# Kernel optimization log

Measured on AMD Instinct MI355X. Metric: run time of the kernel, lower is better.

The kernel has to match this reference:

```python
import math
import jax, jax.numpy as jnp
import numpy as np

B, N, D_IN, D_MODEL, H, TOPK = 4, 2048, 256, 512, 8, 32
D_HEAD = D_MODEL // H
EPS = 1e-8


def _linear_params(key, fan_in, fan_out):
    lim = 1.0 / math.sqrt(fan_in)
    kw, kb = jax.random.split(key)
    W = jax.random.uniform(kw, (fan_in, fan_out), minval=-lim, maxval=lim, dtype=jnp.float32)
    b = jax.random.uniform(kb, (fan_out,), minval=-lim, maxval=lim, dtype=jnp.float32)
    return W, b


def setup_inputs() -> dict:
    key = jax.random.key(0)
    kx, ks, kq, kk, kv, ko = jax.random.split(key, 6)
    x = jax.random.normal(kx, (B, N, D_IN), dtype=jnp.float32)
    sim = jax.random.uniform(ks, (B, N, N), dtype=jnp.float32)  # non-negative similarity
    Wq, bq = _linear_params(kq, D_IN, D_MODEL)
    Wk, bk = _linear_params(kk, D_IN, D_MODEL)
    Wv, bv = _linear_params(kv, D_IN, D_MODEL)
    Wo, bo = _linear_params(ko, D_MODEL, D_MODEL)
    tau_raw = jnp.asarray(0.0, dtype=jnp.float32)
    return {"x": x, "sim": sim, "Wq": Wq, "bq": bq, "Wk": Wk, "bk": bk,
            "Wv": Wv, "bv": bv, "Wo": Wo, "bo": bo, "tau_raw": tau_raw}


def reference(x, sim, Wq, bq, Wk, bk, Wv, bv, Wo, bo, tau_raw):
    b, n, _ = x.shape
    # projections -> (B, H, N, d_head)
    def split_heads(t):
        return t.reshape(b, n, H, D_HEAD).transpose(0, 2, 1, 3)
    Qh = split_heads(x @ Wq + bq)
    Kh = split_heads(x @ Wk + bk)
    Vh = split_heads(x @ Wv + bv)

    # top-k masked, row-normalized similarity bias
    simc = jnp.maximum(sim, 0.0)
    diag = jnp.eye(n, dtype=bool)
    sim_for_topk = jnp.where(diag, -jnp.inf, simc)  # exclude self from top-k
    k = min(TOPK, n - 1)
    _, topk_idx = jax.lax.top_k(sim_for_topk, k)  # (B, N, k)
    bidx = jnp.arange(b)[:, None, None]
    ridx = jnp.arange(n)[None, :, None]
    keep = jnp.zeros((b, n, n), dtype=bool).at[bidx, ridx, topk_idx].set(True)
    keep = keep & ~diag
    sim_masked = jnp.where(keep, simc, 0.0)
    rowsum = jnp.maximum(sim_masked.sum(axis=-1, keepdims=True), EPS)
    sim_bias = sim_masked / rowsum  # (B, N, N), rows sum to 1 over kept entries

    tau = jax.nn.softplus(tau_raw)
    scale = 1.0 / math.sqrt(D_HEAD)
    logits = jnp.einsum('bhnd,bhmd->bhnm', Qh, Kh) * scale + tau * sim_bias[:, None, :, :]
    attn = jax.nn.softmax(logits, axis=-1)
    out = jnp.einsum('bhnm,bhmd->bhnd', attn, Vh)
    out = out.transpose(0, 2, 1, 3).reshape(b, n, D_MODEL)
    return out @ Wo + bo
```

## Files before the change

kernel.cpp:

```cpp
#include <hip/hip_runtime.h>

typedef unsigned int u32;
typedef unsigned short u16;
typedef unsigned long long u64;
typedef float f32x4 __attribute__((ext_vector_type(4)));
typedef u32 u32x4 __attribute__((ext_vector_type(4)));
typedef u32 u32x2 __attribute__((ext_vector_type(2)));

#define DEVINL static __device__ __forceinline__
#define LOG2E 1.44269504088896340736f
#define QSCALE 0.18033688011112042f

DEVINL u16 f2bf(float f) {
  u32 u = __builtin_bit_cast(u32, f);
  u32 r = u + 0x7FFFu + ((u >> 16) & 1u);
  return (u16)(r >> 16);
}

DEVINL u32 cvtpk(float lo, float hi) {
  u32 r;
  asm("v_cvt_pk_bf16_f32 %0, %1, %2" : "=v"(r) : "v"(lo), "v"(hi));
  return r;
}
DEVINL float exp2v(float x) {
  float r;
  asm("v_exp_f32 %0, %1" : "=v"(r) : "v"(x));
  return r;
}
DEVINL void mfma_b16(f32x4& c, u32x4 a, u32x4 b) {
  asm volatile("v_mfma_f32_16x16x32_bf16 %0, %1, %2, %0" : "+v"(c) : "v"(a), "v"(b));
}
DEVINL void mfma_fence() { asm volatile("s_nop 7\n\ts_nop 7"); }

DEVINL int mbcnt64(u64 m) {
  return __builtin_amdgcn_mbcnt_hi((u32)(m >> 32), __builtin_amdgcn_mbcnt_lo((u32)m, 0));
}
DEVINL u64 shfl_xor64(u64 v, int m) {
  u32 lo = (u32)v, hi = (u32)(v >> 32);
  lo = __shfl_xor(lo, m, 64);
  hi = __shfl_xor(hi, m, 64);
  return ((u64)hi << 32) | lo;
}

__global__ __launch_bounds__(256) void prep_kernel(
    const float* __restrict__ x, const float* __restrict__ Wq, const float* __restrict__ Wk,
    const float* __restrict__ Wv, const float* __restrict__ Wo, const float* __restrict__ bq,
    const float* __restrict__ bk, const float* __restrict__ bv, u16* __restrict__ xb,
    u16* __restrict__ WqkvT, u16* __restrict__ WoT, float* __restrict__ biasQKV) {
  __shared__ float T[64][65];
  const int blk = blockIdx.x, tid = threadIdx.x;
  if (blk < 1024) {
    int i0 = (blk * 256 + tid) * 8;
    f32x4 v0 = *(const f32x4*)(x + i0);
    f32x4 v1 = *(const f32x4*)(x + i0 + 4);
    u32x4 pk;
    pk[0] = (u32)f2bf(v0[0]) | ((u32)f2bf(v0[1]) << 16);
    pk[1] = (u32)f2bf(v0[2]) | ((u32)f2bf(v0[3]) << 16);
    pk[2] = (u32)f2bf(v1[0]) | ((u32)f2bf(v1[1]) << 16);
    pk[3] = (u32)f2bf(v1[2]) | ((u32)f2bf(v1[3]) << 16);
    *(u32x4*)(xb + i0) = pk;
    return;
  }
  if (blk < 1024 + 96 + 64) {
    int t = blk - 1024;
    const float* W;
    u16* dst;
    int k0, n0, outld, outrow0;
    if (t < 96) {
      int sel = t >> 5, tt = t & 31;
      W = sel == 0 ? Wq : (sel == 1 ? Wk : Wv);
      k0 = (tt >> 3) * 64;
      n0 = (tt & 7) * 64;
      dst = WqkvT;
      outld = 256;
      outrow0 = sel * 512 + n0;
    } else {
      int tt = t - 96;
      W = Wo;
      k0 = (tt >> 3) * 64;
      n0 = (tt & 7) * 64;
      dst = WoT;
      outld = 512;
      outrow0 = n0;
    }
    const int r = tid >> 2, q = tid & 3;
#pragma unroll
    for (int i = 0; i < 4; i++) {
      f32x4 vv = *(const f32x4*)(W + (size_t)(k0 + r) * 512 + n0 + q * 16 + i * 4);
      T[r][q * 16 + i * 4 + 0] = vv[0];
      T[r][q * 16 + i * 4 + 1] = vv[1];
      T[r][q * 16 + i * 4 + 2] = vv[2];
      T[r][q * 16 + i * 4 + 3] = vv[3];
    }
    __syncthreads();
    u16 tmpv[16];
#pragma unroll
    for (int e = 0; e < 16; e++) tmpv[e] = f2bf(T[q * 16 + e][r]);
    u32x4 w0, w1;
#pragma unroll
    for (int j = 0; j < 4; j++) {
      w0[j] = (u32)tmpv[2 * j] | ((u32)tmpv[2 * j + 1] << 16);
      w1[j] = (u32)tmpv[8 + 2 * j] | ((u32)tmpv[9 + 2 * j] << 16);
    }
    u16* dp = dst + (size_t)(outrow0 + r) * outld + k0 + q * 16;
    *(u32x4*)dp = w0;
    *(u32x4*)(dp + 8) = w1;
    return;
  }
  for (int i = tid; i < 1536; i += 256)
    biasQKV[i] = i < 512 ? bq[i] : (i < 1024 ? bk[i - 512] : bv[i - 1024]);
}

__global__ __launch_bounds__(256) void topk_kernel(const float* __restrict__ sim,
                                                   const float* __restrict__ tau_raw,
                                                   u32* __restrict__ tpw,
                                                   u32* __restrict__ tstarts) {
  __shared__ u32 keyA[4][64];
  __shared__ u32 idxA[4][64];
  const int tid = threadIdx.x, lane = tid & 63, w = tid >> 6;
  const int row = blockIdx.x * 4 + w;
  const int b = row >> 11, n = row & 2047;
  const float* src = sim + ((size_t)b * 2048 + n) * 2048;

  u32 keys[32];
#pragma unroll
  for (int q = 0; q < 8; q++) {
    f32x4 v = *(const f32x4*)(src + q * 256 + lane * 4);
#pragma unroll
    for (int j = 0; j < 4; j++) {
      int m = (q << 8) + lane * 4 + j;
      float xv = fmaxf(v[j], 0.f);
      keys[q * 4 + j] = (m == n) ? 0u : (__builtin_bit_cast(u32, xv) + 1u);
    }
  }

  u32 Plo = 1u;
  u32 Phi = 0x7F000000u;
  u32 P = 0x3F7C0001u;
  int c = 0;
  for (int it = 0; it < 40; ++it) {
    int lc = 0;
#pragma unroll
    for (int e = 0; e < 32; e++) lc += (keys[e] >= P) ? 1 : 0;
#pragma unroll
    for (int off = 1; off < 64; off <<= 1) lc += __shfl_xor(lc, off, 64);
    c = lc;
    if (c >= 32 && c <= 64) break;
    if (c < 32) Phi = P; else Plo = P;
    if (Phi - Plo <= 1) break;
    long long Pn;
    if (P >= 0x3F000000u && P <= 0x3F800000u) {
      Pn = (long long)P + (long long)(c - 48) * 4098;
    } else {
      Pn = (long long)Plo + (long long)((Phi - Plo) >> 1);
    }
    if (Pn <= (long long)Plo || Pn >= (long long)Phi)
      Pn = (long long)Plo + (long long)((Phi - Plo) >> 1);
    P = (u32)Pn;
  }

  u32* kws = keyA[w];
  u32* iws = idxA[w];
  int base = 0;
#pragma unroll
  for (int e = 0; e < 32; e++) {
    bool pred = keys[e] >= P;
    u64 mk = __ballot(pred);
    if (pred) {
      int slot = base + mbcnt64(mk);
      if (slot < 64) {
        kws[slot] = keys[e];
        iws[slot] = (u32)((e >> 2) * 256 + lane * 4 + (e & 3));
      }
    }
    base += __popcll(mk);
  }
  for (int s = base + lane; s < 64; s += 64) {
    kws[s] = 0u;
    iws[s] = 2047u;
  }

  u64 K = ((u64)kws[lane] << 11) | (u64)(2047u - iws[lane]);
#pragma unroll
  for (int k = 2; k <= 64; k <<= 1) {
#pragma unroll
    for (int j = k >> 1; j >= 1; j >>= 1) {
      u64 o = shfl_xor64(K, j);
      bool keepmax = (((lane & k) == 0) == ((lane & j) == 0));
      u64 mx = K > o ? K : o;
      u64 mn = K > o ? o : K;
      K = keepmax ? mx : mn;
    }
  }

  u32 key = (u32)(K >> 11);
  int myidx = 2047 - (int)(K & 0x7FFu);
  float myval = __builtin_bit_cast(float, key - 1u);
  float sv = (lane < 32) ? myval : 0.f;
#pragma unroll
  for (int off = 1; off < 64; off <<= 1) sv += __shfl_xor(sv, off, 64);
  float tau = log1pf(__expf(tau_raw[0]));
  float wvv = tau * myval / fmaxf(sv, 1e-8f) * LOG2E;

  int bucket = (myidx >> 2) & 3;
  u64 bm0 = __ballot(lane < 32 && bucket == 0);
  u64 bm1 = __ballot(lane < 32 && bucket == 1);
  u64 bm2 = __ballot(lane < 32 && bucket == 2);
  int c0 = __popcll(bm0), c1 = __popcll(bm1), c2 = __popcll(bm2);
  int key2 = (bucket << 11) | myidx;
  int rank = 0;
  for (int j2 = 0; j2 < 32; j2++) {
    int ok = __shfl(key2, j2, 64);
    rank += (ok < key2) ? 1 : 0;
  }
  if (lane < 32) tpw[(size_t)row * 32 + rank] = ((u32)myidx << 16) | (u32)f2bf(wvv);
  if (lane == 0)
    tstarts[row] = ((u32)c0 << 8) | ((u32)(c0 + c1) << 16) | ((u32)(c0 + c1 + c2) << 24);
}

template <int MODE>
__global__ __launch_bounds__(256) void gemm_nt(const u16* __restrict__ A,
                                               const u16* __restrict__ Bt,
                                               const float* __restrict__ bias,
                                               u16* __restrict__ outQ, u16* __restrict__ outK,
                                               u16* __restrict__ outV, float* __restrict__ outF,
                                               int M, int N, int K) {
  __shared__ __align__(16) u16 As[128 * 32];
  __shared__ __align__(16) u16 Bs[128 * 32];

  const int tid = threadIdx.x;
  const int lane = tid & 63;
  const int w = tid >> 6;
  const int g = lane >> 4, c = lane & 15;
  const int wr = (w >> 1) * 64, wc = (w & 1) * 64;
  const int m0 = blockIdx.y * 128, n0 = blockIdx.x * 128;

  f32x4 acc[4][4];
#pragma unroll
  for (int i = 0; i < 4; i++)
#pragma unroll
    for (int j = 0; j < 4; j++) acc[i][j] = f32x4{0.f, 0.f, 0.f, 0.f};

  const int srow = tid >> 1;
  const int shalf = tid & 1;
  const u16* Arow = A + (size_t)(m0 + srow) * K + shalf * 16;
  const u16* Brow = Bt + (size_t)(n0 + srow) * K + shalf * 16;
  char* asbase = (char*)As;
  char* bsbase = (char*)Bs;
  const u32 swz = (u32)((srow & 7) << 4);
  const u32 wb0 = (u32)(srow * 64 + shalf * 32);

  for (int kt = 0; kt < K; kt += 32) {
    __syncthreads();
    {
      u32x4 a0 = *(const u32x4*)(Arow + kt);
      u32x4 a1 = *(const u32x4*)(Arow + kt + 8);
      u32x4 b0 = *(const u32x4*)(Brow + kt);
      u32x4 b1 = *(const u32x4*)(Brow + kt + 8);
      *(u32x4*)(asbase + ((wb0 + 0) ^ swz)) = a0;
      *(u32x4*)(asbase + ((wb0 + 16) ^ swz)) = a1;
      *(u32x4*)(bsbase + ((wb0 + 0) ^ swz)) = b0;
      *(u32x4*)(bsbase + ((wb0 + 16) ^ swz)) = b1;
    }
    __syncthreads();
    u32x4 af[4], bfr[4];
#pragma unroll
    for (int fr = 0; fr < 4; fr++) {
      int row = wr + fr * 16 + c;
      af[fr] = *(const u32x4*)(asbase + ((u32)(row * 64 + g * 16) ^ ((u32)((row & 7) << 4))));
    }
#pragma unroll
    for (int fc = 0; fc < 4; fc++) {
      int row = wc + fc * 16 + c;
      bfr[fc] = *(const u32x4*)(bsbase + ((u32)(row * 64 + g * 16) ^ ((u32)((row & 7) << 4))));
    }
#pragma unroll
    for (int fr = 0; fr < 4; fr++)
#pragma unroll
      for (int fc = 0; fc < 4; fc++) mfma_b16(acc[fr][fc], af[fr], bfr[fc]);
  }
  mfma_fence();
#pragma unroll
  for (int fc = 0; fc < 4; fc++) {
    int gcol = n0 + wc + fc * 16 + c;
    float bvv = bias[gcol];
#pragma unroll
    for (int fr = 0; fr < 4; fr++) {
#pragma unroll
      for (int r = 0; r < 4; r++) {
        int grow = m0 + wr + fr * 16 + 4 * g + r;
        float v = acc[fr][fc][r] + bvv;
        if (MODE == 0) {
          int sel = gcol >> 9, c9 = gcol & 511;
          if (sel == 0) v *= QSCALE;
          int hh = c9 >> 6, dd = c9 & 63;
          int bb = grow >> 11, nn = grow & 2047;
          size_t off2 = ((size_t)(bb * 8 + hh) * 2048 + nn) * 64 + dd;
          u16* dst = sel == 0 ? outQ : (sel == 1 ? outK : outV);
          dst[off2] = f2bf(v);
        } else {
          outF[(size_t)grow * N + gcol] = v;
        }
      }
    }
  }
}

__global__ __launch_bounds__(256) void transpose_v(const u16* __restrict__ Vb,
                                                   u16* __restrict__ Vt) {
  __shared__ __align__(16) u16 T[64 * 72];
  const int nt = blockIdx.x, bh = blockIdx.y;
  const int tid = threadIdx.x;
  const int rr = tid >> 2, q = tid & 3;
  {
    const u16* src = Vb + ((size_t)bh * 2048 + nt * 64 + rr) * 64 + q * 16;
    u32x4 a = *(const u32x4*)src;
    u32x4 b = *(const u32x4*)(src + 8);
    *(u32x4*)(&T[rr * 72 + q * 16]) = a;
    *(u32x4*)(&T[rr * 72 + q * 16 + 8]) = b;
  }
  __syncthreads();
  {
    union { u16 s[16]; u32x4 v[2]; } ou;
#pragma unroll
    for (int e = 0; e < 16; e++) ou.s[e] = T[(q * 16 + e) * 72 + rr];
    u16* dst = Vt + ((size_t)bh * 64 + rr) * 2048 + nt * 64 + q * 16;
    *(u32x4*)dst = ou.v[0];
    *(u32x4*)(dst + 8) = ou.v[1];
  }
}

__global__ __launch_bounds__(256) void attn_kernel(const u16* __restrict__ Qb,
                                                   const u16* __restrict__ Kb,
                                                   const u16* __restrict__ Vt,
                                                   const u32* __restrict__ tpw,
                                                   const u32* __restrict__ tstarts,
                                                   u16* __restrict__ attnout) {
  __shared__ __align__(16) u16 Ks[64 * 64];
  __shared__ __align__(16) u16 Vs[64 * 64];
  __shared__ __align__(16) u16 Ps[4][16 * 64];
  __shared__ u32 pws[64 * 32];
  __shared__ u32 tst[64];

  const int bid = blockIdx.x;
  const int bh = (bid & 7) * 4 + ((bid >> 3) & 3);
  const int qt = bid >> 5;
  const int b = bh >> 3, h = bh & 7;
  const int tid = threadIdx.x, lane = tid & 63, w = tid >> 6;
  const int g = lane >> 4, c = lane & 15;
  const int qbase = qt * 64;

  for (int i = tid; i < 2048; i += 256)
    pws[i] = tpw[((size_t)b * 2048 + qbase) * 32 + i];
  if (tid < 64) tst[tid] = tstarts[b * 2048 + qbase + tid];

  const u16* qptr = Qb + ((size_t)bh * 2048 + qbase + w * 16 + c) * 64 + g * 8;
  u32x4 aq0 = *(const u32x4*)qptr;
  u32x4 aq1 = *(const u32x4*)(qptr + 32);

  float m = -1e30f, ssum = 0.f;
  f32x4 o[4];
#pragma unroll
  for (int db = 0; db < 4; db++) o[db] = f32x4{0.f, 0.f, 0.f, 0.f};

  const int rowl = w * 16 + c;

  const int sr = tid >> 2, sq = tid & 3;
  const u16* ksrc = Kb + ((size_t)bh * 2048 + sr) * 64 + sq * 16;
  const u16* vsrc = Vt + ((size_t)bh * 64 + sr) * 2048 + sq * 16;
  char* ksb = (char*)Ks;
  char* vsb = (char*)Vs;
  char* pwb = (char*)&Ps[w][0];
  const u32 sswz = (u32)((sr & 7) << 4);
  const u32 sb0 = (u32)(sr * 128 + sq * 32);

  u32 koff[4][2], poff2[2], pwoff[4][2];
#pragma unroll
  for (int cb = 0; cb < 4; cb++) {
    int row = cb * 16 + c;
    u32 sz = (u32)((row & 7) << 4);
    koff[cb][0] = ((u32)(row * 128 + g * 16)) ^ sz;
    koff[cb][1] = ((u32)(row * 128 + g * 16 + 64)) ^ sz;
  }
  {
    u32 sz = (u32)((c & 7) << 4);
#pragma unroll
    for (int mm = 0; mm < 2; mm++) poff2[mm] = ((u32)(c * 128 + mm * 64 + g * 16)) ^ sz;
#pragma unroll
    for (int cb = 0; cb < 4; cb++)
#pragma unroll
      for (int hh = 0; hh < 2; hh++)
        pwoff[cb][hh] = ((u32)(c * 128 + cb * 32 + g * 8 + hh * 4)) ^ sz;
  }

  __syncthreads();
  u32 stw = tst[rowl];
  int p = (int)((stw >> (8 * g)) & 255u);
  const int pend = (g == 3) ? 32 : (int)((stw >> (8 * g + 8)) & 255u);

  for (int jt = 0; jt < 2048; jt += 64) {
    __syncthreads();
    {
      u32x4 k0 = *(const u32x4*)(ksrc + (size_t)jt * 64);
      u32x4 k1 = *(const u32x4*)(ksrc + (size_t)jt * 64 + 8);
      u32x4 v0 = *(const u32x4*)(vsrc + jt);
      u32x4 v1 = *(const u32x4*)(vsrc + jt + 8);
      *(u32x4*)(ksb + ((sb0 + 0) ^ sswz)) = k0;
      *(u32x4*)(ksb + ((sb0 + 16) ^ sswz)) = k1;
      *(u32x4*)(vsb + ((sb0 + 0) ^ sswz)) = v0;
      *(u32x4*)(vsb + ((sb0 + 16) ^ sswz)) = v1;
    }
    __syncthreads();

    f32x4 s[4];
#pragma unroll
    for (int cb = 0; cb < 4; cb++) {
      u32x4 bk0 = *(const u32x4*)(ksb + koff[cb][0]);
      u32x4 bk1 = *(const u32x4*)(ksb + koff[cb][1]);
      f32x4 t = f32x4{0.f, 0.f, 0.f, 0.f};
      mfma_b16(t, bk0, aq0);
      mfma_b16(t, bk1, aq1);
      s[cb] = t;
    }
    mfma_fence();

    const int jtend = jt + 64;
    while (p < pend) {
      u32 e = pws[rowl * 32 + p];
      int j = (int)(e >> 16);
      if (j >= jtend) break;
      float wv = __builtin_bit_cast(float, e << 16);
      int rel = j - jt - 4 * g;
#pragma unroll
      for (int cb = 0; cb < 4; cb++)
#pragma unroll
        for (int r = 0; r < 4; r++) s[cb][r] += (rel == cb * 16 + r) ? wv : 0.f;
      p++;
    }

    float tm = fmaxf(fmaxf(fmaxf(s[0][0], s[0][1]), fmaxf(s[0][2], s[0][3])),
                     fmaxf(fmaxf(s[1][0], s[1][1]), fmaxf(s[1][2], s[1][3])));
    tm = fmaxf(tm, fmaxf(fmaxf(fmaxf(s[2][0], s[2][1]), fmaxf(s[2][2], s[2][3])),
                         fmaxf(fmaxf(s[3][0], s[3][1]), fmaxf(s[3][2], s[3][3]))));
    tm = fmaxf(tm, __shfl_xor(tm, 16, 64));
    tm = fmaxf(tm, __shfl_xor(tm, 32, 64));
    if (!__all(tm - m <= 8.f)) {
      float mn = fmaxf(m, tm);
      float f = exp2v(m - mn);
      m = mn;
      ssum *= f;
#pragma unroll
      for (int db = 0; db < 4; db++) o[db] *= f;
    }
    float lsum = 0.f;
#pragma unroll
    for (int cb = 0; cb < 4; cb++) {
      float e0 = exp2v(s[cb][0] - m);
      float e1 = exp2v(s[cb][1] - m);
      float e2 = exp2v(s[cb][2] - m);
      float e3 = exp2v(s[cb][3] - m);
      lsum += (e0 + e1) + (e2 + e3);
      *(u32*)(pwb + pwoff[cb][0]) = cvtpk(e0, e1);
      *(u32*)(pwb + pwoff[cb][1]) = cvtpk(e2, e3);
    }
    ssum += lsum;

    u32x4 pf0 = *(const u32x4*)(pwb + poff2[0]);
    u32x4 pf1 = *(const u32x4*)(pwb + poff2[1]);
#pragma unroll
    for (int db = 0; db < 4; db++) {
      u32x4 bv0 = *(const u32x4*)(vsb + koff[db][0]);
      u32x4 bv1 = *(const u32x4*)(vsb + koff[db][1]);
      mfma_b16(o[db], bv0, pf0);
      mfma_b16(o[db], bv1, pf1);
    }
    mfma_fence();
  }

  ssum += __shfl_xor(ssum, 16, 64);
  ssum += __shfl_xor(ssum, 32, 64);
  float inv = 1.f / ssum;
  const int n = qbase + w * 16 + c;
  u16* obase = attnout + ((size_t)b * 2048 + n) * 512 + h * 64 + 4 * g;
#pragma unroll
  for (int db = 0; db < 4; db++) {
    u32x2 st;
    st[0] = cvtpk(o[db][0] * inv, o[db][1] * inv);
    st[1] = cvtpk(o[db][2] * inv, o[db][3] * inv);
    *(u32x2*)(obase + db * 16) = st;
  }
}

extern "C" void kernel_launch(void* const* d_in, const int* in_sizes, int n_in,
                              void* d_out, int out_size, void* d_ws, size_t ws_size,
                              hipStream_t stream) {
  (void)in_sizes; (void)n_in; (void)out_size; (void)ws_size;
  const float* x = (const float*)d_in[0];
  const float* sim = (const float*)d_in[1];
  const float* Wq = (const float*)d_in[2];
  const float* bq = (const float*)d_in[3];
  const float* Wk = (const float*)d_in[4];
  const float* bk = (const float*)d_in[5];
  const float* Wv = (const float*)d_in[6];
  const float* bv = (const float*)d_in[7];
  const float* Wo = (const float*)d_in[8];
  const float* bo = (const float*)d_in[9];
  const float* tau = (const float*)d_in[10];
  float* out = (float*)d_out;

  char* ws = (char*)d_ws;
  size_t off = 0;
  auto alloc = [&](size_t bytes) {
    void* p = ws + off;
    off += (bytes + 255) & ~(size_t)255;
    return p;
  };
  u16* xb = (u16*)alloc((size_t)8192 * 256 * 2);
  u16* WqkvT = (u16*)alloc((size_t)1536 * 256 * 2);
  u16* WoT = (u16*)alloc((size_t)512 * 512 * 2);
  float* biasQKV = (float*)alloc((size_t)1536 * 4);
  u16* Qb = (u16*)alloc((size_t)32 * 2048 * 64 * 2);
  u16* Kb = (u16*)alloc((size_t)32 * 2048 * 64 * 2);
  u16* Vb = (u16*)alloc((size_t)32 * 2048 * 64 * 2);
  u16* Vt = (u16*)alloc((size_t)32 * 2048 * 64 * 2);
  u16* attnout = (u16*)alloc((size_t)8192 * 512 * 2);
  u32* tpw = (u32*)alloc((size_t)8192 * 32 * 4);
  u32* tstarts = (u32*)alloc((size_t)8192 * 4);

  prep_kernel<<<dim3(1185), dim3(256), 0, stream>>>(x, Wq, Wk, Wv, Wo, bq, bk, bv, xb, WqkvT,
                                                    WoT, biasQKV);
  topk_kernel<<<dim3(2048), dim3(256), 0, stream>>>(sim, tau, tpw, tstarts);
  gemm_nt<0><<<dim3(12, 64), dim3(256), 0, stream>>>(xb, WqkvT, biasQKV, Qb, Kb, Vb, nullptr,
                                                     8192, 1536, 256);
  transpose_v<<<dim3(32, 32), dim3(256), 0, stream>>>(Vb, Vt);
  attn_kernel<<<dim3(1024), dim3(256), 0, stream>>>(Qb, Kb, Vt, tpw, tstarts, attnout);
  gemm_nt<1><<<dim3(4, 64), dim3(256), 0, stream>>>(attnout, WoT, bo, nullptr, nullptr, nullptr,
                                                    out, 8192, 512, 512);
}
```

Measured before the change: 256.5 us.

## Double-buffer K/V tiles and process two query sub-tiles per attention block

The attention kernel now handles 128 query rows per block (two 64-row sub-tiles per wave), so each K/V tile loaded into shared memory is reused for twice as many queries. K/V staging becomes double-buffered with register prefetch two tiles ahead, which removes one barrier per iteration and overlaps global loads with MFMA work. The probability tile writes are also widened to 64-bit stores. The cost is more registers and shared memory per block and half as many blocks (512), which may lower occupancy and leave fewer blocks to spread across the GPU's CUs.

```diff
diff --git a/kernel.cpp b/kernel.cpp
--- a/kernel.cpp
+++ b/kernel.cpp
@@ -336,11 +336,11 @@
                                                    const u32* __restrict__ tpw,
                                                    const u32* __restrict__ tstarts,
                                                    u16* __restrict__ attnout) {
-  __shared__ __align__(16) u16 Ks[64 * 64];
-  __shared__ __align__(16) u16 Vs[64 * 64];
-  __shared__ __align__(16) u16 Ps[4][16 * 64];
-  __shared__ u32 pws[64 * 32];
-  __shared__ u32 tst[64];
+  __shared__ __align__(16) u16 Kd[2][64 * 64];
+  __shared__ __align__(16) u16 Vd[2][64 * 64];
+  __shared__ __align__(16) u16 Ps[4][2][16 * 64];
+  __shared__ u32 pws[128 * 32];
+  __shared__ u32 tst[128];
 
   const int bid = blockIdx.x;
   const int bh = (bid & 7) * 4 + ((bid >> 3) & 3);
@@ -348,33 +348,36 @@
   const int b = bh >> 3, h = bh & 7;
   const int tid = threadIdx.x, lane = tid & 63, w = tid >> 6;
   const int g = lane >> 4, c = lane & 15;
-  const int qbase = qt * 64;
-
-  for (int i = tid; i < 2048; i += 256)
+  const int qbase = qt * 128;
+
+  for (int i = tid; i < 4096; i += 256)
     pws[i] = tpw[((size_t)b * 2048 + qbase) * 32 + i];
-  if (tid < 64) tst[tid] = tstarts[b * 2048 + qbase + tid];
-
-  const u16* qptr = Qb + ((size_t)bh * 2048 + qbase + w * 16 + c) * 64 + g * 8;
-  u32x4 aq0 = *(const u32x4*)qptr;
-  u32x4 aq1 = *(const u32x4*)(qptr + 32);
-
-  float m = -1e30f, ssum = 0.f;
-  f32x4 o[4];
-#pragma unroll
-  for (int db = 0; db < 4; db++) o[db] = f32x4{0.f, 0.f, 0.f, 0.f};
-
-  const int rowl = w * 16 + c;
+  if (tid < 128) tst[tid] = tstarts[b * 2048 + qbase + tid];
+
+  u32x4 aq0[2], aq1[2];
+#pragma unroll
+  for (int s = 0; s < 2; s++) {
+    const u16* qptr = Qb + ((size_t)bh * 2048 + qbase + s * 64 + w * 16 + c) * 64 + g * 8;
+    aq0[s] = *(const u32x4*)qptr;
+    aq1[s] = *(const u32x4*)(qptr + 32);
+  }
+
+  float m[2] = {-1e30f, -1e30f}, ssum[2] = {0.f, 0.f};
+  f32x4 o[2][4];
+#pragma unroll
+  for (int s = 0; s < 2; s++)
+#pragma unroll
+    for (int db = 0; db < 4; db++) o[s][db] = f32x4{0.f, 0.f, 0.f, 0.f};
 
   const int sr = tid >> 2, sq = tid & 3;
   const u16* ksrc = Kb + ((size_t)bh * 2048 + sr) * 64 + sq * 16;
   const u16* vsrc = Vt + ((size_t)bh * 64 + sr) * 2048 + sq * 16;
-  char* ksb = (char*)Ks;
-  char* vsb = (char*)Vs;
-  char* pwb = (char*)&Ps[w][0];
+  char* ksbase = (char*)&Kd[0][0];
+  char* vsbase = (char*)&Vd[0][0];
   const u32 sswz = (u32)((sr & 7) << 4);
   const u32 sb0 = (u32)(sr * 128 + sq * 32);
 
-  u32 koff[4][2], poff2[2], pwoff[4][2];
+  u32 koff[4][2];
 #pragma unroll
   for (int cb = 0; cb < 4; cb++) {
     int row = cb * 16 + c;
@@ -382,112 +385,163 @@
     koff[cb][0] = ((u32)(row * 128 + g * 16)) ^ sz;
     koff[cb][1] = ((u32)(row * 128 + g * 16 + 64)) ^ sz;
   }
+  u32 poff2[2], pwoff[4];
   {
     u32 sz = (u32)((c & 7) << 4);
 #pragma unroll
     for (int mm = 0; mm < 2; mm++) poff2[mm] = ((u32)(c * 128 + mm * 64 + g * 16)) ^ sz;
 #pragma unroll
-    for (int cb = 0; cb < 4; cb++)
-#pragma unroll
-      for (int hh = 0; hh < 2; hh++)
-        pwoff[cb][hh] = ((u32)(c * 128 + cb * 32 + g * 8 + hh * 4)) ^ sz;
-  }
-
+    for (int cb = 0; cb < 4; cb++) pwoff[cb] = ((u32)(c * 128 + cb * 32 + g * 8)) ^ sz;
+  }
+
+  int p[2], pend[2];
+
+  u32x4 rk0 = *(const u32x4*)(ksrc);
+  u32x4 rk1 = *(const u32x4*)(ksrc + 8);
+  u32x4 rv0 = *(const u32x4*)(vsrc);
+  u32x4 rv1 = *(const u32x4*)(vsrc + 8);
+  *(u32x4*)(ksbase + ((sb0 + 0) ^ sswz)) = rk0;
+  *(u32x4*)(ksbase + ((sb0 + 16) ^ sswz)) = rk1;
+  *(u32x4*)(vsbase + ((sb0 + 0) ^ sswz)) = rv0;
+  *(u32x4*)(vsbase + ((sb0 + 16) ^ sswz)) = rv1;
+  rk0 = *(const u32x4*)(ksrc + 4096);
+  rk1 = *(const u32x4*)(ksrc + 4096 + 8);
+  rv0 = *(const u32x4*)(vsrc + 64);
+  rv1 = *(const u32x4*)(vsrc + 64 + 8);
   __syncthreads();
-  u32 stw = tst[rowl];
-  int p = (int)((stw >> (8 * g)) & 255u);
-  const int pend = (g == 3) ? 32 : (int)((stw >> (8 * g + 8)) & 255u);
-
-  for (int jt = 0; jt < 2048; jt += 64) {
+
+#pragma unroll
+  for (int s = 0; s < 2; s++) {
+    u32 stw = tst[s * 64 + w * 16 + c];
+    p[s] = (int)((stw >> (8 * g)) & 255u);
+    pend[s] = (g == 3) ? 32 : (int)((stw >> (8 * g + 8)) & 255u);
+  }
+
+  u32 curoff = 0;
+  for (int t = 0; t < 32; ++t) {
+    const int jt = t * 64;
+    {
+      u32 woff = curoff ^ 8192;
+      *(u32x4*)(ksbase + woff + ((sb0 + 0) ^ sswz)) = rk0;
+      *(u32x4*)(ksbase + woff + ((sb0 + 16) ^ sswz)) = rk1;
+      *(u32x4*)(vsbase + woff + ((sb0 + 0) ^ sswz)) = rv0;
+      *(u32x4*)(vsbase + woff + ((sb0 + 16) ^ sswz)) = rv1;
+    }
+    {
+      int jt2 = t < 30 ? (t + 2) * 64 : 1984;
+      const u16* kp = ksrc + (size_t)jt2 * 64;
+      const u16* vp = vsrc + jt2;
+      rk0 = *(const u32x4*)kp;
+      rk1 = *(const u32x4*)(kp + 8);
+      rv0 = *(const u32x4*)vp;
+      rv1 = *(const u32x4*)(vp + 8);
+    }
+
+    f32x4 sA[4], sB[4];
+#pragma unroll
+    for (int cb = 0; cb < 4; cb++) {
+      u32x4 bk0 = *(const u32x4*)(ksbase + curoff + koff[cb][0]);
+      u32x4 bk1 = *(const u32x4*)(ksbase + curoff + koff[cb][1]);
+      f32x4 tA = f32x4{0.f, 0.f, 0.f, 0.f};
+      f32x4 tB = f32x4{0.f, 0.f, 0.f, 0.f};
+      mfma_b16(tA, bk0, aq0[0]);
+      mfma_b16(tA, bk1, aq1[0]);
+      mfma_b16(tB, bk0, aq0[1]);
+      mfma_b16(tB, bk1, aq1[1]);
+      sA[cb] = tA;
+      sB[cb] = tB;
+    }
+    mfma_fence();
+
+    const int jtend = jt + 64;
+#pragma unroll
+    for (int s = 0; s < 2; s++) {
+      f32x4* sp = (s == 0) ? sA : sB;
+      const int rowl = s * 64 + w * 16 + c;
+      int pp = p[s];
+      const int pe = pend[s];
+      while (pp < pe) {
+        u32 e = pws[rowl * 32 + pp];
+        int j = (int)(e >> 16);
+        if (j >= jtend) break;
+        float wv = __builtin_bit_cast(float, e << 16);
+        int rel = j - jt - 4 * g;
+#pragma unroll
+        for (int cb = 0; cb < 4; cb++)
+#pragma unroll
+          for (int r = 0; r < 4; r++) sp[cb][r] += (rel == cb * 16 + r) ? wv : 0.f;
+        pp++;
+      }
+      p[s] = pp;
+
+      float tm = fmaxf(fmaxf(fmaxf(sp[0][0], sp[0][1]), fmaxf(sp[0][2], sp[0][3])),
+                       fmaxf(fmaxf(sp[1][0], sp[1][1]), fmaxf(sp[1][2], sp[1][3])));
+      tm = fmaxf(tm, fmaxf(fmaxf(fmaxf(sp[2][0], sp[2][1]), fmaxf(sp[2][2], sp[2][3])),
+                           fmaxf(fmaxf(sp[3][0], sp[3][1]), fmaxf(sp[3][2], sp[3][3]))));
+      tm = fmaxf(tm, __shfl_xor(tm, 16, 64));
+      tm = fmaxf(tm, __shfl_xor(tm, 32, 64));
+      if (!__all(tm - m[s] <= 8.f)) {
+        float mn = fmaxf(m[s], tm);
+        float f = exp2v(m[s] - mn);
+        m[s] = mn;
+        ssum[s] *= f;
+#pragma unroll
+        for (int db = 0; db < 4; db++) o[s][db] *= f;
+      }
+      char* pwb = (char*)&Ps[w][s][0];
+      float lsum = 0.f;
+#pragma unroll
+      for (int cb = 0; cb < 4; cb++) {
+        float e0 = exp2v(sp[cb][0] - m[s]);
+        float e1 = exp2v(sp[cb][1] - m[s]);
+        float e2 = exp2v(sp[cb][2] - m[s]);
+        float e3 = exp2v(sp[cb][3] - m[s]);
+        lsum += (e0 + e1) + (e2 + e3);
+        u32x2 pk;
+        pk[0] = cvtpk(e0, e1);
+        pk[1] = cvtpk(e2, e3);
+        *(u32x2*)(pwb + pwoff[cb]) = pk;
+      }
+      ssum[s] += lsum;
+    }
+
+    char* pwbA = (char*)&Ps[w][0][0];
+    char* pwbB = (char*)&Ps[w][1][0];
+    u32x4 pf0A = *(const u32x4*)(pwbA + poff2[0]);
+    u32x4 pf1A = *(const u32x4*)(pwbA + poff2[1]);
+    u32x4 pf0B = *(const u32x4*)(pwbB + poff2[0]);
+    u32x4 pf1B = *(const u32x4*)(pwbB + poff2[1]);
+
+#pragma unroll
+    for (int db = 0; db < 4; db++) {
+      u32x4 bv0 = *(const u32x4*)(vsbase + curoff + koff[db][0]);
+      u32x4 bv1 = *(const u32x4*)(vsbase + curoff + koff[db][1]);
+      mfma_b16(o[0][db], bv0, pf0A);
+      mfma_b16(o[0][db], bv1, pf1A);
+      mfma_b16(o[1][db], bv0, pf0B);
+      mfma_b16(o[1][db], bv1, pf1B);
+    }
+    mfma_fence();
+
     __syncthreads();
-    {
-      u32x4 k0 = *(const u32x4*)(ksrc + (size_t)jt * 64);
-      u32x4 k1 = *(const u32x4*)(ksrc + (size_t)jt * 64 + 8);
-      u32x4 v0 = *(const u32x4*)(vsrc + jt);
-      u32x4 v1 = *(const u32x4*)(vsrc + jt + 8);
-      *(u32x4*)(ksb + ((sb0 + 0) ^ sswz)) = k0;
-      *(u32x4*)(ksb + ((sb0 + 16) ^ sswz)) = k1;
-      *(u32x4*)(vsb + ((sb0 + 0) ^ sswz)) = v0;
-      *(u32x4*)(vsb + ((sb0 + 16) ^ sswz)) = v1;
-    }
-    __syncthreads();
-
-    f32x4 s[4];
-#pragma unroll
-    for (int cb = 0; cb < 4; cb++) {
-      u32x4 bk0 = *(const u32x4*)(ksb + koff[cb][0]);
-      u32x4 bk1 = *(const u32x4*)(ksb + koff[cb][1]);
-      f32x4 t = f32x4{0.f, 0.f, 0.f, 0.f};
-      mfma_b16(t, bk0, aq0);
-      mfma_b16(t, bk1, aq1);
-      s[cb] = t;
-    }
-    mfma_fence();
-
-    const int jtend = jt + 64;
-    while (p < pend) {
-      u32 e = pws[rowl * 32 + p];
-      int j = (int)(e >> 16);
-      if (j >= jtend) break;
-      float wv = __builtin_bit_cast(float, e << 16);
-      int rel = j - jt - 4 * g;
-#pragma unroll
-      for (int cb = 0; cb < 4; cb++)
-#pragma unroll
-        for (int r = 0; r < 4; r++) s[cb][r] += (rel == cb * 16 + r) ? wv : 0.f;
-      p++;
-    }
-
-    float tm = fmaxf(fmaxf(fmaxf(s[0][0], s[0][1]), fmaxf(s[0][2], s[0][3])),
-                     fmaxf(fmaxf(s[1][0], s[1][1]), fmaxf(s[1][2], s[1][3])));
-    tm = fmaxf(tm, fmaxf(fmaxf(fmaxf(s[2][0], s[2][1]), fmaxf(s[2][2], s[2][3])),
-                         fmaxf(fmaxf(s[3][0], s[3][1]), fmaxf(s[3][2], s[3][3]))));
-    tm = fmaxf(tm, __shfl_xor(tm, 16, 64));
-    tm = fmaxf(tm, __shfl_xor(tm, 32, 64));
-    if (!__all(tm - m <= 8.f)) {
-      float mn = fmaxf(m, tm);
-      float f = exp2v(m - mn);
-      m = mn;
-      ssum *= f;
-#pragma unroll
-      for (int db = 0; db < 4; db++) o[db] *= f;
-    }
-    float lsum = 0.f;
-#pragma unroll
-    for (int cb = 0; cb < 4; cb++) {
-      float e0 = exp2v(s[cb][0] - m);
-      float e1 = exp2v(s[cb][1] - m);
-      float e2 = exp2v(s[cb][2] - m);
-      float e3 = exp2v(s[cb][3] - m);
-      lsum += (e0 + e1) + (e2 + e3);
-      *(u32*)(pwb + pwoff[cb][0]) = cvtpk(e0, e1);
-      *(u32*)(pwb + pwoff[cb][1]) = cvtpk(e2, e3);
-    }
-    ssum += lsum;
-
-    u32x4 pf0 = *(const u32x4*)(pwb + poff2[0]);
-    u32x4 pf1 = *(const u32x4*)(pwb + poff2[1]);
+    curoff ^= 8192;
+  }
+
+#pragma unroll
+  for (int s = 0; s < 2; s++) {
+    float t = ssum[s];
+    t += __shfl_xor(t, 16, 64);
+    t += __shfl_xor(t, 32, 64);
+    float inv = 1.f / t;
+    const int n = qbase + s * 64 + w * 16 + c;
+    u16* obase = attnout + ((size_t)b * 2048 + n) * 512 + h * 64 + 4 * g;
 #pragma unroll
     for (int db = 0; db < 4; db++) {
-      u32x4 bv0 = *(const u32x4*)(vsb + koff[db][0]);
-      u32x4 bv1 = *(const u32x4*)(vsb + koff[db][1]);
-      mfma_b16(o[db], bv0, pf0);
-      mfma_b16(o[db], bv1, pf1);
-    }
-    mfma_fence();
-  }
-
-  ssum += __shfl_xor(ssum, 16, 64);
-  ssum += __shfl_xor(ssum, 32, 64);
-  float inv = 1.f / ssum;
-  const int n = qbase + w * 16 + c;
-  u16* obase = attnout + ((size_t)b * 2048 + n) * 512 + h * 64 + 4 * g;
-#pragma unroll
-  for (int db = 0; db < 4; db++) {
-    u32x2 st;
-    st[0] = cvtpk(o[db][0] * inv, o[db][1] * inv);
-    st[1] = cvtpk(o[db][2] * inv, o[db][3] * inv);
-    *(u32x2*)(obase + db * 16) = st;
+      u32x2 st;
+      st[0] = cvtpk(o[s][db][0] * inv, o[s][db][1] * inv);
+      st[1] = cvtpk(o[s][db][2] * inv, o[s][db][3] * inv);
+      *(u32x2*)(obase + db * 16) = st;
+    }
   }
 }
 
@@ -533,7 +587,7 @@
   gemm_nt<0><<<dim3(12, 64), dim3(256), 0, stream>>>(xb, WqkvT, biasQKV, Qb, Kb, Vb, nullptr,
                                                      8192, 1536, 256);
   transpose_v<<<dim3(32, 32), dim3(256), 0, stream>>>(Vb, Vt);
-  attn_kernel<<<dim3(1024), dim3(256), 0, stream>>>(Qb, Kb, Vt, tpw, tstarts, attnout);
+  attn_kernel<<<dim3(512), dim3(256), 0, stream>>>(Qb, Kb, Vt, tpw, tstarts, attnout);
   gemm_nt<1><<<dim3(4, 64), dim3(256), 0, stream>>>(attnout, WoT, bo, nullptr, nullptr, nullptr,
                                                     out, 8192, 512, 512);
 }
```

Measured after the change: 272.3 us. 1.06x slower.

## Prefetch next K/V tile into registers and stream top-k bias from global

Applied to the files above, without the earlier changes.

The attention loop now loads the next K/V tile into registers while the current tile is computed, so global latency overlaps with the MFMA and softmax work. The per-block shared-memory staging of top-k weights and start indices is removed; each lane instead reads its next sparse entry straight from global memory using a one-entry lookahead. It also merges two 32-bit P stores into one 64-bit store, adds s_setprio around the MFMA sections, and drops the fence after the PV MFMAs inside the loop. The trade-offs are higher register pressure from holding the prefetched tile and scattered global loads in the bias loop.

```diff
diff --git a/kernel.cpp b/kernel.cpp
--- a/kernel.cpp
+++ b/kernel.cpp
@@ -339,8 +339,6 @@
   __shared__ __align__(16) u16 Ks[64 * 64];
   __shared__ __align__(16) u16 Vs[64 * 64];
   __shared__ __align__(16) u16 Ps[4][16 * 64];
-  __shared__ u32 pws[64 * 32];
-  __shared__ u32 tst[64];
 
   const int bid = blockIdx.x;
   const int bh = (bid & 7) * 4 + ((bid >> 3) & 3);
@@ -349,21 +347,22 @@
   const int tid = threadIdx.x, lane = tid & 63, w = tid >> 6;
   const int g = lane >> 4, c = lane & 15;
   const int qbase = qt * 64;
-
-  for (int i = tid; i < 2048; i += 256)
-    pws[i] = tpw[((size_t)b * 2048 + qbase) * 32 + i];
-  if (tid < 64) tst[tid] = tstarts[b * 2048 + qbase + tid];
-
-  const u16* qptr = Qb + ((size_t)bh * 2048 + qbase + w * 16 + c) * 64 + g * 8;
+  const int rowl = w * 16 + c;
+
+  const u16* qptr = Qb + ((size_t)bh * 2048 + qbase + rowl) * 64 + g * 8;
   u32x4 aq0 = *(const u32x4*)qptr;
   u32x4 aq1 = *(const u32x4*)(qptr + 32);
 
+  const u32* tpwrow = tpw + ((size_t)b * 2048 + qbase + rowl) * 32;
+  u32 stw = tstarts[b * 2048 + qbase + rowl];
+  int p = (int)((stw >> (8 * g)) & 255u);
+  const int pend = (g == 3) ? 32 : (int)((stw >> (8 * g + 8)) & 255u);
+  u32 nextE = (p < pend) ? tpwrow[p] : 0xFFFF0000u;
+
   float m = -1e30f, ssum = 0.f;
   f32x4 o[4];
 #pragma unroll
   for (int db = 0; db < 4; db++) o[db] = f32x4{0.f, 0.f, 0.f, 0.f};
-
-  const int rowl = w * 16 + c;
 
   const int sr = tid >> 2, sq = tid & 3;
   const u16* ksrc = Kb + ((size_t)bh * 2048 + sr) * 64 + sq * 16;
@@ -374,7 +373,7 @@
   const u32 sswz = (u32)((sr & 7) << 4);
   const u32 sb0 = (u32)(sr * 128 + sq * 32);
 
-  u32 koff[4][2], poff2[2], pwoff[4][2];
+  u32 koff[4][2], poff2[2], pwoff[4];
 #pragma unroll
   for (int cb = 0; cb < 4; cb++) {
     int row = cb * 16 + c;
@@ -387,55 +386,57 @@
 #pragma unroll
     for (int mm = 0; mm < 2; mm++) poff2[mm] = ((u32)(c * 128 + mm * 64 + g * 16)) ^ sz;
 #pragma unroll
-    for (int cb = 0; cb < 4; cb++)
-#pragma unroll
-      for (int hh = 0; hh < 2; hh++)
-        pwoff[cb][hh] = ((u32)(c * 128 + cb * 32 + g * 8 + hh * 4)) ^ sz;
-  }
-
-  __syncthreads();
-  u32 stw = tst[rowl];
-  int p = (int)((stw >> (8 * g)) & 255u);
-  const int pend = (g == 3) ? 32 : (int)((stw >> (8 * g + 8)) & 255u);
-
-  for (int jt = 0; jt < 2048; jt += 64) {
+    for (int cb = 0; cb < 4; cb++) pwoff[cb] = ((u32)(c * 128 + cb * 32 + g * 8)) ^ sz;
+  }
+
+  u32x4 rk0 = *(const u32x4*)ksrc;
+  u32x4 rk1 = *(const u32x4*)(ksrc + 8);
+  u32x4 rv0 = *(const u32x4*)vsrc;
+  u32x4 rv1 = *(const u32x4*)(vsrc + 8);
+
+  for (int t = 0; t < 32; ++t) {
+    const int jt = t * 64;
     __syncthreads();
+    *(u32x4*)(ksb + ((sb0 + 0) ^ sswz)) = rk0;
+    *(u32x4*)(ksb + ((sb0 + 16) ^ sswz)) = rk1;
+    *(u32x4*)(vsb + ((sb0 + 0) ^ sswz)) = rv0;
+    *(u32x4*)(vsb + ((sb0 + 16) ^ sswz)) = rv1;
+    __syncthreads();
+
     {
-      u32x4 k0 = *(const u32x4*)(ksrc + (size_t)jt * 64);
-      u32x4 k1 = *(const u32x4*)(ksrc + (size_t)jt * 64 + 8);
-      u32x4 v0 = *(const u32x4*)(vsrc + jt);
-      u32x4 v1 = *(const u32x4*)(vsrc + jt + 8);
-      *(u32x4*)(ksb + ((sb0 + 0) ^ sswz)) = k0;
-      *(u32x4*)(ksb + ((sb0 + 16) ^ sswz)) = k1;
-      *(u32x4*)(vsb + ((sb0 + 0) ^ sswz)) = v0;
-      *(u32x4*)(vsb + ((sb0 + 16) ^ sswz)) = v1;
-    }
-    __syncthreads();
-
+      int jt2 = t < 31 ? jt + 64 : 1984;
+      const u16* kp = ksrc + (size_t)jt2 * 64;
+      const u16* vp = vsrc + jt2;
+      rk0 = *(const u32x4*)kp;
+      rk1 = *(const u32x4*)(kp + 8);
+      rv0 = *(const u32x4*)vp;
+      rv1 = *(const u32x4*)(vp + 8);
+    }
+
+    __builtin_amdgcn_s_setprio(1);
     f32x4 s[4];
 #pragma unroll
     for (int cb = 0; cb < 4; cb++) {
       u32x4 bk0 = *(const u32x4*)(ksb + koff[cb][0]);
       u32x4 bk1 = *(const u32x4*)(ksb + koff[cb][1]);
-      f32x4 t = f32x4{0.f, 0.f, 0.f, 0.f};
-      mfma_b16(t, bk0, aq0);
-      mfma_b16(t, bk1, aq1);
-      s[cb] = t;
-    }
+      f32x4 tacc = f32x4{0.f, 0.f, 0.f, 0.f};
+      mfma_b16(tacc, bk0, aq0);
+      mfma_b16(tacc, bk1, aq1);
+      s[cb] = tacc;
+    }
+    __builtin_amdgcn_s_setprio(0);
     mfma_fence();
 
     const int jtend = jt + 64;
-    while (p < pend) {
-      u32 e = pws[rowl * 32 + p];
-      int j = (int)(e >> 16);
-      if (j >= jtend) break;
-      float wv = __builtin_bit_cast(float, e << 16);
-      int rel = j - jt - 4 * g;
+    while ((int)(nextE >> 16) < jtend) {
+      float wv = __builtin_bit_cast(float, nextE << 16);
+      int rel = (int)(nextE >> 16) - jt - 4 * g;
 #pragma unroll
       for (int cb = 0; cb < 4; cb++)
 #pragma unroll
         for (int r = 0; r < 4; r++) s[cb][r] += (rel == cb * 16 + r) ? wv : 0.f;
       p++;
+      nextE = (p < pend) ? tpwrow[p] : 0xFFFF0000u;
     }
 
     float tm = fmaxf(fmaxf(fmaxf(s[0][0], s[0][1]), fmaxf(s[0][2], s[0][3])),
@@ -460,13 +461,16 @@
       float e2 = exp2v(s[cb][2] - m);
       float e3 = exp2v(s[cb][3] - m);
       lsum += (e0 + e1) + (e2 + e3);
-      *(u32*)(pwb + pwoff[cb][0]) = cvtpk(e0, e1);
-      *(u32*)(pwb + pwoff[cb][1]) = cvtpk(e2, e3);
+      u32x2 pk;
+      pk[0] = cvtpk(e0, e1);
+      pk[1] = cvtpk(e2, e3);
+      *(u32x2*)(pwb + pwoff[cb]) = pk;
     }
     ssum += lsum;
 
     u32x4 pf0 = *(const u32x4*)(pwb + poff2[0]);
     u32x4 pf1 = *(const u32x4*)(pwb + poff2[1]);
+    __builtin_amdgcn_s_setprio(1);
 #pragma unroll
     for (int db = 0; db < 4; db++) {
       u32x4 bv0 = *(const u32x4*)(vsb + koff[db][0]);
@@ -474,13 +478,14 @@
       mfma_b16(o[db], bv0, pf0);
       mfma_b16(o[db], bv1, pf1);
     }
-    mfma_fence();
-  }
+    __builtin_amdgcn_s_setprio(0);
+  }
+  mfma_fence();
 
   ssum += __shfl_xor(ssum, 16, 64);
   ssum += __shfl_xor(ssum, 32, 64);
   float inv = 1.f / ssum;
-  const int n = qbase + w * 16 + c;
+  const int n = qbase + rowl;
   u16* obase = attnout + ((size_t)b * 2048 + n) * 512 + h * 64 + 4 * g;
 #pragma unroll
   for (int db = 0; db < 4; db++) {
```

After: 250.5 us. 1.02x faster.
